# Optimization experiments

Hardware: AMD Instinct MI355X
Metric: run time of the kernel (lower is better)

Reference implementation:

```python
import jax, jax.numpy as jnp
import numpy as np

N, E = 50000, 800000
NFEAT, NHID, NCLASS = 128, 64, 40
GROUPS = 32  # min(32, nhid)
EPS = 1e-5


def _gcn(x, W, b, src, tgt, mvals):
    # GraphConvolution: linear, gather from src, weighted scatter-add to tgt
    s = x @ W + b                                  # [N, out]
    msg = s[src] * mvals[:, None]                   # [E, out]
    return jax.ops.segment_sum(msg, tgt, num_segments=N)


def _groupnorm(x, gamma, beta):
    n, c = x.shape
    xg = x.reshape(n, GROUPS, c // GROUPS)
    mu = jnp.mean(xg, axis=-1, keepdims=True)
    var = jnp.mean(jnp.square(xg - mu), axis=-1, keepdims=True)
    xn = ((xg - mu) * jax.lax.rsqrt(var + EPS)).reshape(n, c)
    return xn * gamma + beta


def setup_inputs() -> dict:
    key = jax.random.key(0)
    ks = jax.random.split(key, 16)
    x = jax.random.normal(ks[0], (N, NFEAT), dtype=jnp.float32)
    src = jax.random.randint(ks[1], (E,), 0, N, dtype=jnp.int64)
    tgt = jax.random.randint(ks[2], (E,), 0, N, dtype=jnp.int64)
    Mtgt = jax.random.uniform(ks[3], (E,), dtype=jnp.float32)

    def glorot(k, fin, fout):
        lim = np.sqrt(6.0 / (fin + fout))
        return jax.random.uniform(k, (fin, fout), jnp.float32, -lim, lim)

    return {
        "x": x, "src": src, "tgt": tgt, "Mtgt": Mtgt,
        "W0": glorot(ks[4], NFEAT, NHID), "b0": jnp.zeros((NHID,), jnp.float32),
        "W1": glorot(ks[5], NHID, NHID),  "b1": jnp.zeros((NHID,), jnp.float32),
        "W2": glorot(ks[6], NHID, NHID),  "b2": jnp.zeros((NHID,), jnp.float32),
        "W3": glorot(ks[7], NHID, NCLASS),"b3": jnp.zeros((NCLASS,), jnp.float32),
        "g1": jnp.ones((NHID,), jnp.float32), "beta1": jnp.zeros((NHID,), jnp.float32),
        "g2": jnp.ones((NHID,), jnp.float32), "beta2": jnp.zeros((NHID,), jnp.float32),
    }


def reference(x, src, tgt, Mtgt, W0, b0, W1, b1, W2, b2, W3, b3, g1, beta1, g2, beta2):
    # layer 0 + relu (dropout is identity in eval mode)
    h = jax.nn.relu(_gcn(x, W0, b0, src, tgt, Mtgt))
    # middle layers: residue_layers=1 -> each layer is its own residual block
    r = h
    h = _groupnorm(jax.nn.relu(_gcn(h, W1, b1, src, tgt, Mtgt)), g1, beta1) + r
    r = h
    h = _groupnorm(jax.nn.relu(_gcn(h, W2, b2, src, tgt, Mtgt)), g2, beta2) + r
    # output layer
    h = _gcn(h, W3, b3, src, tgt, Mtgt)
    return jax.nn.log_softmax(h, axis=1)
```

## Files before the change

kernel.cpp:

```cpp
#include <hip/hip_runtime.h>
#include <hip/hip_bf16.h>
#include <hip/hip_fp16.h>
#include <math.h>


#define EPS 1e-5f
#define ELLC 48
#define CPAD 4
#define NPART 8

__device__ inline unsigned pack_h2(float a, float b) {
    __half2 h = __floats2half2_rn(a, b);
    return *(unsigned*)&h;
}
__device__ inline float2 unpack_h2(unsigned u) {
    __half2 h = *(__half2*)&u;
    return __half22float2(h);
}
__device__ inline float h16f(unsigned short u) {
    __half h;
    *(unsigned short*)&h = u;
    return __half2float(h);
}

__global__ void fill_lin0_kernel(const int* __restrict__ src,
                                 const int* __restrict__ tgt,
                                 const float* __restrict__ mv,
                                 int* __restrict__ cntp,
                                 unsigned* __restrict__ ep, int E,
                                 const float* __restrict__ X,
                                 const float4* __restrict__ W4,
                                 const float4* __restrict__ B4,
                                 uint2* __restrict__ ShOut, int n, int psz,
                                 int fillBlocks, int halfBlocks) {
    __shared__ float4 Wl[128 * 8];
    __shared__ float4 Bl8[8];
    if (blockIdx.x < (unsigned)fillBlocks) {
        int part = blockIdx.x & (NPART - 1);
        int chunk = blockIdx.x >> 3;
        int e = chunk * blockDim.x + threadIdx.x;
        if (e >= E) return;
        int t = tgt[e];
        if ((unsigned)(t - part * psz) >= (unsigned)psz) return;
        int slot = atomicAdd(&cntp[t * CPAD], 1);
        if (slot < ELLC) {
            __half hw = __float2half_rn(mv[e]);
            unsigned v = (unsigned)src[e] |
                         ((unsigned)*(unsigned short*)&hw << 16);
            ep[(long)t * ELLC + slot] = v;
        }
        return;
    }
    int tb = blockIdx.x - fillBlocks;
    int half = (tb >= halfBlocks) ? 1 : 0;
    int bi = tb - half * halfBlocks;
    for (int i = threadIdx.x; i < 128 * 8; i += blockDim.x)
        Wl[i] = W4[(i >> 3) * 16 + half * 8 + (i & 7)];
    if (threadIdx.x < 8) Bl8[threadIdx.x] = B4[half * 8 + threadIdx.x];
    __syncthreads();
    int idx = bi * blockDim.x + threadIdx.x;
    if (idx >= n * 8) return;
    int row = idx >> 3;
    int c8 = idx & 7;
    const float* xr = X + (long)row * 128;
    float4 acc = Bl8[c8];
#pragma unroll 8
    for (int k = 0; k < 128; ++k) {
        float xv = xr[k];
        float4 w = Wl[k * 8 + c8];
        acc.x = fmaf(xv, w.x, acc.x);
        acc.y = fmaf(xv, w.y, acc.y);
        acc.z = fmaf(xv, w.z, acc.z);
        acc.w = fmaf(xv, w.w, acc.w);
    }
    ShOut[(long)row * 16 + half * 8 + c8] =
        make_uint2(pack_h2(acc.x, acc.y), pack_h2(acc.z, acc.w));
}

#define FMA4(A, V, W4)                                                        \
    A.x = fmaf(V.x, W4, A.x); A.y = fmaf(V.y, W4, A.y);                       \
    A.z = fmaf(V.z, W4, A.z); A.w = fmaf(V.w, W4, A.w);

#define HF_FMA(A, U, WV) {                                                    \
    float2 _lo = unpack_h2(U.x), _hi = unpack_h2(U.y);                        \
    A.x = fmaf(_lo.x, WV, A.x); A.y = fmaf(_lo.y, WV, A.y);                   \
    A.z = fmaf(_hi.x, WV, A.z); A.w = fmaf(_hi.y, WV, A.w); }

#define AGG4H_BODY(R2)                                                        \
    int beg = wid * ELLC;                                                     \
    int cnv = cntp[wid * CPAD];                                               \
    if (cnv > ELLC) cnv = ELLC;                                               \
    int end = beg + cnv;                                                      \
    float4 a0 = make_float4(0.f, 0.f, 0.f, 0.f), a1 = a0, a2 = a0, a3 = a0;   \
    int j = beg;                                                              \
    for (; j + 16 <= end; j += 16) {                                          \
        unsigned p0 = ep[j + q], p1 = ep[j + 4 + q];                          \
        unsigned p2 = ep[j + 8 + q], p3 = ep[j + 12 + q];                     \
        uint2 u0 = Sh[(long)(p0 & 0xFFFFu) * R2 + sub];                       \
        uint2 u1 = Sh[(long)(p1 & 0xFFFFu) * R2 + sub];                       \
        uint2 u2 = Sh[(long)(p2 & 0xFFFFu) * R2 + sub];                       \
        uint2 u3 = Sh[(long)(p3 & 0xFFFFu) * R2 + sub];                       \
        float w0 = h16f((unsigned short)(p0 >> 16));                          \
        float w1 = h16f((unsigned short)(p1 >> 16));                          \
        float w2 = h16f((unsigned short)(p2 >> 16));                          \
        float w3 = h16f((unsigned short)(p3 >> 16));                          \
        HF_FMA(a0, u0, w0) HF_FMA(a1, u1, w1)                                 \
        HF_FMA(a2, u2, w2) HF_FMA(a3, u3, w3)                                 \
    }                                                                         \
    for (; j + 4 <= end; j += 4) {                                            \
        unsigned p0 = ep[j + q];                                              \
        uint2 u0 = Sh[(long)(p0 & 0xFFFFu) * R2 + sub];                       \
        float w0 = h16f((unsigned short)(p0 >> 16));                          \
        HF_FMA(a0, u0, w0)                                                    \
    }                                                                         \
    if (j < end) {                                                            \
        int eidx = j + q;                                                     \
        unsigned p0 = ep[(eidx < end) ? eidx : (end - 1)];                    \
        uint2 u0 = Sh[(long)(p0 & 0xFFFFu) * R2 + sub];                       \
        float w0 = (eidx < end) ? h16f((unsigned short)(p0 >> 16)) : 0.f;     \
        HF_FMA(a0, u0, w0)                                                    \
    }                                                                         \
    float4 acc;                                                               \
    acc.x = (a0.x + a1.x) + (a2.x + a3.x);                                    \
    acc.y = (a0.y + a1.y) + (a2.y + a3.y);                                    \
    acc.z = (a0.z + a1.z) + (a2.z + a3.z);                                    \
    acc.w = (a0.w + a1.w) + (a2.w + a3.w);                                    \
    acc.x += __shfl_xor(acc.x, 16); acc.y += __shfl_xor(acc.y, 16);           \
    acc.z += __shfl_xor(acc.z, 16); acc.w += __shfl_xor(acc.w, 16);           \
    acc.x += __shfl_xor(acc.x, 32); acc.y += __shfl_xor(acc.y, 32);           \
    acc.z += __shfl_xor(acc.z, 32); acc.w += __shfl_xor(acc.w, 32);

#define LIN_TAIL_CORE(C4OUT)                                                  \
    float4 o = make_float4(0.f, 0.f, 0.f, 0.f);                               \
    {                                                                         \
        const float* hr = hrow[w];                                            \
        _Pragma("unroll")                                                     \
        for (int kk = 0; kk < 16; ++kk) {                                     \
            float hv = hr[16 * q + kk];                                       \
            float4 wv = Wl[(16 * q + kk) * C4OUT + sub];                      \
            FMA4(o, wv, hv)                                                   \
        }                                                                     \
        o.x += __shfl_xor(o.x, 16); o.y += __shfl_xor(o.y, 16);               \
        o.z += __shfl_xor(o.z, 16); o.w += __shfl_xor(o.w, 16);               \
        o.x += __shfl_xor(o.x, 32); o.y += __shfl_xor(o.y, 32);               \
        o.z += __shfl_xor(o.z, 32); o.w += __shfl_xor(o.w, 32);               \
    }

__global__ void agg_relu_lin_kernel(const uint2* __restrict__ Sh,
                                    const int* __restrict__ cntp,
                                    const unsigned* __restrict__ ep,
                                    const float4* __restrict__ W4,
                                    const float4* __restrict__ B4,
                                    float4* __restrict__ H4,
                                    uint2* __restrict__ ShOut, int n) {
    __shared__ float4 Wl[64 * 16];
    __shared__ float4 Bl[16];
    __shared__ float hrow[4][64];
    for (int i = threadIdx.x; i < 64 * 16; i += blockDim.x) Wl[i] = W4[i];
    if (threadIdx.x < 16) Bl[threadIdx.x] = B4[threadIdx.x];
    __syncthreads();
    int wid = (blockIdx.x * blockDim.x + threadIdx.x) >> 6;
    int lane = threadIdx.x & 63;
    int q = lane >> 4, sub = lane & 15;
    int w = threadIdx.x >> 6;
    if (wid >= n) return;
    AGG4H_BODY(16)
    if (q == 0) {
        float4 h = make_float4(fmaxf(acc.x, 0.f), fmaxf(acc.y, 0.f),
                               fmaxf(acc.z, 0.f), fmaxf(acc.w, 0.f));
        H4[(long)wid * 16 + sub] = h;
        ((float4*)hrow[w])[sub] = h;
    }
    LIN_TAIL_CORE(16)
    if (q == 0) {
        float4 b = Bl[sub];
        o.x += b.x; o.y += b.y; o.z += b.z; o.w += b.w;
        ShOut[(long)wid * 16 + sub] =
            make_uint2(pack_h2(o.x, o.y), pack_h2(o.z, o.w));
    }
}

template <int C4OUT>
__global__ void agg_gn_lin_kernel(const uint2* __restrict__ Sh,
                                  const int* __restrict__ cntp,
                                  const unsigned* __restrict__ ep,
                                  const float4* __restrict__ gamma,
                                  const float4* __restrict__ beta,
                                  const float4* __restrict__ W4,
                                  const float4* __restrict__ B4,
                                  float4* __restrict__ H4,
                                  uint2* __restrict__ ShOut, int n) {
    __shared__ float4 Wl[64 * C4OUT];
    __shared__ float4 Bl[C4OUT];
    __shared__ float hrow[4][64];
    for (int i = threadIdx.x; i < 64 * C4OUT; i += blockDim.x) Wl[i] = W4[i];
    if (threadIdx.x < C4OUT) Bl[threadIdx.x] = B4[threadIdx.x];
    __syncthreads();
    int wid = (blockIdx.x * blockDim.x + threadIdx.x) >> 6;
    int lane = threadIdx.x & 63;
    int q = lane >> 4, sub = lane & 15;
    int w = threadIdx.x >> 6;
    if (wid >= n) return;
    AGG4H_BODY(16)
    if (q == 0) {
        float p0 = fmaxf(acc.x, 0.f), p1 = fmaxf(acc.y, 0.f);
        float p2 = fmaxf(acc.z, 0.f), p3 = fmaxf(acc.w, 0.f);
        float dA = 0.5f * (p0 - p1);
        float dB = 0.5f * (p2 - p3);
        float rsA = rsqrtf(dA * dA + EPS);
        float rsB = rsqrtf(dB * dB + EPS);
        float4 g = gamma[sub], be = beta[sub];
        long off = (long)wid * 16 + sub;
        float4 h = H4[off];
        h.x += dA * rsA * g.x + be.x;
        h.y += -dA * rsA * g.y + be.y;
        h.z += dB * rsB * g.z + be.z;
        h.w += -dB * rsB * g.w + be.w;
        H4[off] = h;
        ((float4*)hrow[w])[sub] = h;
    }
    if (sub < C4OUT) {
        LIN_TAIL_CORE(C4OUT)
        if (q == 0) {
            float4 b = Bl[sub];
            o.x += b.x; o.y += b.y; o.z += b.z; o.w += b.w;
            ShOut[(long)wid * C4OUT + sub] =
                make_uint2(pack_h2(o.x, o.y), pack_h2(o.z, o.w));
        }
    }
}

__global__ void agg_lsm_kernel(const uint2* __restrict__ Sh,
                               const int* __restrict__ cntp,
                               const unsigned* __restrict__ ep,
                               float4* __restrict__ out4, int n) {
    int wid = (blockIdx.x * blockDim.x + threadIdx.x) >> 6;
    int lane = threadIdx.x & 63;
    int q = lane >> 4;
    int sub0 = lane & 15;
    int sub = (sub0 < 10) ? sub0 : 9;
    if (wid >= n) return;
    AGG4H_BODY(10)
    bool valid = sub0 < 10;
    float m = valid ? fmaxf(fmaxf(acc.x, acc.y), fmaxf(acc.z, acc.w)) : -INFINITY;
#pragma unroll
    for (int mk = 8; mk; mk >>= 1) m = fmaxf(m, __shfl_xor(m, mk));
    float ex = valid ? (expf(acc.x - m) + expf(acc.y - m) +
                        expf(acc.z - m) + expf(acc.w - m)) : 0.f;
#pragma unroll
    for (int mk = 8; mk; mk >>= 1) ex += __shfl_xor(ex, mk);
    float l = m + logf(ex);
    if (q == 0 && valid)
        out4[(long)wid * 10 + sub0] =
            make_float4(acc.x - l, acc.y - l, acc.z - l, acc.w - l);
}

extern "C" void kernel_launch(void* const* d_in, const int* in_sizes, int n_in,
                              void* d_out, int out_size, void* d_ws,
                              size_t ws_size, hipStream_t stream) {
    const float* x = (const float*)d_in[0];
    const int* src = (const int*)d_in[1];
    const int* tgt = (const int*)d_in[2];
    const float* mv = (const float*)d_in[3];
    const float* W0 = (const float*)d_in[4];
    const float* b0 = (const float*)d_in[5];
    const float* W1 = (const float*)d_in[6];
    const float* b1 = (const float*)d_in[7];
    const float* W2 = (const float*)d_in[8];
    const float* b2 = (const float*)d_in[9];
    const float* W3 = (const float*)d_in[10];
    const float* b3 = (const float*)d_in[11];
    const float* g1 = (const float*)d_in[12];
    const float* beta1 = (const float*)d_in[13];
    const float* g2 = (const float*)d_in[14];
    const float* beta2 = (const float*)d_in[15];

    const int N = in_sizes[0] / 128;
    const int E = in_sizes[1];

    uint2* bufA = (uint2*)d_ws;
    float* buf_h = (float*)(bufA + (size_t)N * 16);
    uint2* bufB = (uint2*)(buf_h + (size_t)N * 64);
    int* cntp = (int*)(bufB + (size_t)N * 16);
    unsigned* epack = (unsigned*)(((uintptr_t)(cntp + (size_t)N * CPAD) + 15) &
                                  ~(uintptr_t)15);

    const int BLK = 256;
    auto grid = [](long total, int blk) { return (int)((total + blk - 1) / blk); };
    const int chunkBlocks = grid(E, BLK);
    const int fillBlocks = NPART * chunkBlocks;
    const int halfBlocks = grid((long)N * 8, BLK);
    const int psz = (N + NPART - 1) / NPART;

    hipMemsetAsync(cntp, 0, (size_t)N * CPAD * sizeof(int), stream);
    fill_lin0_kernel<<<fillBlocks + 2 * halfBlocks, BLK, 0, stream>>>(
        src, tgt, mv, cntp, epack, E, x, (const float4*)W0, (const float4*)b0,
        bufA, N, psz, fillBlocks, halfBlocks);

    const int aggBlocks = grid((long)N * 64, BLK);

    agg_relu_lin_kernel<<<aggBlocks, BLK, 0, stream>>>(
        bufA, cntp, epack, (const float4*)W1, (const float4*)b1,
        (float4*)buf_h, bufB, N);

    agg_gn_lin_kernel<16><<<aggBlocks, BLK, 0, stream>>>(
        bufB, cntp, epack, (const float4*)g1, (const float4*)beta1,
        (const float4*)W2, (const float4*)b2, (float4*)buf_h, bufA, N);

    agg_gn_lin_kernel<10><<<aggBlocks, BLK, 0, stream>>>(
        bufA, cntp, epack, (const float4*)g2, (const float4*)beta2,
        (const float4*)W3, (const float4*)b3, (float4*)buf_h, bufB, N);

    agg_lsm_kernel<<<aggBlocks, BLK, 0, stream>>>(
        bufB, cntp, epack, (float4*)d_out, N);
}
```

Before: 298.3 us.

## Split 64-wide gather-aggregation into two column-half passes for cache locality

The fp16 node-feature tables are split into separate low and high 32-column halves, and each aggregation layer now runs as two kernels. Each kernel gathers only one half, so its random-access working set (about 3.2 MB) is more likely to stay cache-resident. The second pass fuses the GroupNorm/residual for its half and the following linear layer. The cost is extra kernel launches, a second traversal of the edge lists, and an extra read and write of H per layer.

Measured after the change: 343.2 us. +15.1%, slower.

```diff
diff --git a/kernel.cpp b/kernel.cpp
--- a/kernel.cpp
+++ b/kernel.cpp
@@ -1,5 +1,4 @@
 #include <hip/hip_runtime.h>
-#include <hip/hip_bf16.h>
 #include <hip/hip_fp16.h>
 #include <math.h>
 
@@ -22,6 +21,15 @@
     *(unsigned short*)&h = u;
     return __half2float(h);
 }
+
+#define FMA4(A, V, W4)                                                        \
+    A.x = fmaf(V.x, W4, A.x); A.y = fmaf(V.y, W4, A.y);                       \
+    A.z = fmaf(V.z, W4, A.z); A.w = fmaf(V.w, W4, A.w);
+
+#define HF_FMA(A, U, WV) {                                                    \
+    float2 _lo = unpack_h2(U.x), _hi = unpack_h2(U.y);                        \
+    A.x = fmaf(_lo.x, WV, A.x); A.y = fmaf(_lo.y, WV, A.y);                   \
+    A.z = fmaf(_hi.x, WV, A.z); A.w = fmaf(_hi.y, WV, A.w); }
 
 __global__ void fill_lin0_kernel(const int* __restrict__ src,
                                  const int* __restrict__ tgt,
@@ -31,7 +39,8 @@
                                  const float* __restrict__ X,
                                  const float4* __restrict__ W4,
                                  const float4* __restrict__ B4,
-                                 uint2* __restrict__ ShOut, int n, int psz,
+                                 uint2* __restrict__ S0lo,
+                                 uint2* __restrict__ S0hi, int n, int psz,
                                  int fillBlocks, int halfBlocks) {
     __shared__ float4 Wl[128 * 8];
     __shared__ float4 Bl8[8];
@@ -73,18 +82,168 @@
         acc.z = fmaf(xv, w.z, acc.z);
         acc.w = fmaf(xv, w.w, acc.w);
     }
-    ShOut[(long)row * 16 + half * 8 + c8] =
-        make_uint2(pack_h2(acc.x, acc.y), pack_h2(acc.z, acc.w));
-}
-
-#define FMA4(A, V, W4)                                                        \
-    A.x = fmaf(V.x, W4, A.x); A.y = fmaf(V.y, W4, A.y);                       \
-    A.z = fmaf(V.z, W4, A.z); A.w = fmaf(V.w, W4, A.w);
-
-#define HF_FMA(A, U, WV) {                                                    \
-    float2 _lo = unpack_h2(U.x), _hi = unpack_h2(U.y);                        \
-    A.x = fmaf(_lo.x, WV, A.x); A.y = fmaf(_lo.y, WV, A.y);                   \
-    A.z = fmaf(_hi.x, WV, A.z); A.w = fmaf(_hi.y, WV, A.w); }
+    uint2 v2 = make_uint2(pack_h2(acc.x, acc.y), pack_h2(acc.z, acc.w));
+    if (half) S0hi[(long)row * 8 + c8] = v2;
+    else      S0lo[(long)row * 8 + c8] = v2;
+}
+
+#define AGGH_BODY()                                                           \
+    int beg = wid * ELLC;                                                     \
+    int cnv = cntp[wid * CPAD];                                               \
+    if (cnv > ELLC) cnv = ELLC;                                               \
+    int end = beg + cnv;                                                      \
+    float4 a0 = make_float4(0.f, 0.f, 0.f, 0.f), a1 = a0;                     \
+    int j = beg;                                                              \
+    for (; j + 16 <= end; j += 16) {                                          \
+        unsigned p0 = ep[j + o], p1 = ep[j + 8 + o];                          \
+        uint2 u0 = Sh[(long)(p0 & 0xFFFFu) * 8 + sub];                        \
+        uint2 u1 = Sh[(long)(p1 & 0xFFFFu) * 8 + sub];                        \
+        float w0 = h16f((unsigned short)(p0 >> 16));                          \
+        float w1 = h16f((unsigned short)(p1 >> 16));                          \
+        HF_FMA(a0, u0, w0) HF_FMA(a1, u1, w1)                                 \
+    }                                                                         \
+    for (; j + 8 <= end; j += 8) {                                            \
+        unsigned p0 = ep[j + o];                                              \
+        uint2 u0 = Sh[(long)(p0 & 0xFFFFu) * 8 + sub];                        \
+        float w0 = h16f((unsigned short)(p0 >> 16));                          \
+        HF_FMA(a0, u0, w0)                                                    \
+    }                                                                         \
+    if (j < end) {                                                            \
+        int eidx = j + o;                                                     \
+        unsigned p0 = ep[(eidx < end) ? eidx : (end - 1)];                    \
+        uint2 u0 = Sh[(long)(p0 & 0xFFFFu) * 8 + sub];                        \
+        float w0 = (eidx < end) ? h16f((unsigned short)(p0 >> 16)) : 0.f;     \
+        HF_FMA(a0, u0, w0)                                                    \
+    }                                                                         \
+    float4 acc;                                                               \
+    acc.x = a0.x + a1.x; acc.y = a0.y + a1.y;                                 \
+    acc.z = a0.z + a1.z; acc.w = a0.w + a1.w;                                 \
+    acc.x += __shfl_xor(acc.x, 8);  acc.y += __shfl_xor(acc.y, 8);            \
+    acc.z += __shfl_xor(acc.z, 8);  acc.w += __shfl_xor(acc.w, 8);            \
+    acc.x += __shfl_xor(acc.x, 16); acc.y += __shfl_xor(acc.y, 16);           \
+    acc.z += __shfl_xor(acc.z, 16); acc.w += __shfl_xor(acc.w, 16);           \
+    acc.x += __shfl_xor(acc.x, 32); acc.y += __shfl_xor(acc.y, 32);           \
+    acc.z += __shfl_xor(acc.z, 32); acc.w += __shfl_xor(acc.w, 32);
+
+__global__ void aggA_relu_kernel(const uint2* __restrict__ Sh,
+                                 const int* __restrict__ cntp,
+                                 const unsigned* __restrict__ ep,
+                                 float4* __restrict__ H4, int n) {
+    int wid = (blockIdx.x * blockDim.x + threadIdx.x) >> 6;
+    int lane = threadIdx.x & 63;
+    int o = lane >> 3, sub = lane & 7;
+    if (wid >= n) return;
+    AGGH_BODY()
+    if (o == 0)
+        H4[(long)wid * 16 + sub] =
+            make_float4(fmaxf(acc.x, 0.f), fmaxf(acc.y, 0.f),
+                        fmaxf(acc.z, 0.f), fmaxf(acc.w, 0.f));
+}
+
+__global__ void aggA_gn_kernel(const uint2* __restrict__ Sh,
+                               const int* __restrict__ cntp,
+                               const unsigned* __restrict__ ep,
+                               const float4* __restrict__ gamma4,
+                               const float4* __restrict__ beta4,
+                               float4* __restrict__ H4, int n) {
+    int wid = (blockIdx.x * blockDim.x + threadIdx.x) >> 6;
+    int lane = threadIdx.x & 63;
+    int o = lane >> 3, sub = lane & 7;
+    if (wid >= n) return;
+    AGGH_BODY()
+    if (o == 0) {
+        float p0 = fmaxf(acc.x, 0.f), p1 = fmaxf(acc.y, 0.f);
+        float p2 = fmaxf(acc.z, 0.f), p3 = fmaxf(acc.w, 0.f);
+        float dA = 0.5f * (p0 - p1);
+        float dB = 0.5f * (p2 - p3);
+        float rsA = rsqrtf(dA * dA + EPS);
+        float rsB = rsqrtf(dB * dB + EPS);
+        float4 g = gamma4[sub], be = beta4[sub];
+        long off = (long)wid * 16 + sub;
+        float4 h = H4[off];
+        h.x += dA * rsA * g.x + be.x;
+        h.y += -dA * rsA * g.y + be.y;
+        h.z += dB * rsB * g.z + be.z;
+        h.w += -dB * rsB * g.w + be.w;
+        H4[off] = h;
+    }
+}
+
+template <int C4OUT, bool SPLIT, bool DOGN>
+__global__ void aggB_kernel(const uint2* __restrict__ Sh,
+                            const int* __restrict__ cntp,
+                            const unsigned* __restrict__ ep,
+                            const float4* __restrict__ gamma4h,
+                            const float4* __restrict__ beta4h,
+                            const float4* __restrict__ W4,
+                            const float4* __restrict__ B4,
+                            float4* __restrict__ H4,
+                            uint2* __restrict__ OutLo,
+                            uint2* __restrict__ OutHi, int n) {
+    __shared__ float4 Wl[64 * C4OUT];
+    __shared__ float4 Bl[C4OUT];
+    __shared__ float hrow[4][64];
+    for (int i = threadIdx.x; i < 64 * C4OUT; i += blockDim.x) Wl[i] = W4[i];
+    if (threadIdx.x < C4OUT) Bl[threadIdx.x] = B4[threadIdx.x];
+    __syncthreads();
+    int wid = (blockIdx.x * blockDim.x + threadIdx.x) >> 6;
+    int lane = threadIdx.x & 63;
+    int o = lane >> 3, sub = lane & 7;
+    int w = threadIdx.x >> 6;
+    if (wid >= n) return;
+    AGGH_BODY()
+    if (o == 1)
+        ((float4*)hrow[w])[sub] = H4[(long)wid * 16 + sub];
+    if (o == 0) {
+        float4 h;
+        long off = (long)wid * 16 + 8 + sub;
+        if (DOGN) {
+            float p0 = fmaxf(acc.x, 0.f), p1 = fmaxf(acc.y, 0.f);
+            float p2 = fmaxf(acc.z, 0.f), p3 = fmaxf(acc.w, 0.f);
+            float dA = 0.5f * (p0 - p1);
+            float dB = 0.5f * (p2 - p3);
+            float rsA = rsqrtf(dA * dA + EPS);
+            float rsB = rsqrtf(dB * dB + EPS);
+            float4 g = gamma4h[sub], be = beta4h[sub];
+            h = H4[off];
+            h.x += dA * rsA * g.x + be.x;
+            h.y += -dA * rsA * g.y + be.y;
+            h.z += dB * rsB * g.z + be.z;
+            h.w += -dB * rsB * g.w + be.w;
+        } else {
+            h = make_float4(fmaxf(acc.x, 0.f), fmaxf(acc.y, 0.f),
+                            fmaxf(acc.z, 0.f), fmaxf(acc.w, 0.f));
+        }
+        H4[off] = h;
+        ((float4*)hrow[w])[8 + sub] = h;
+    }
+    int q16 = lane >> 4, s16 = lane & 15;
+    if (C4OUT == 16 || s16 < C4OUT) {
+        float4 oo = make_float4(0.f, 0.f, 0.f, 0.f);
+        const float* hr = hrow[w];
+#pragma unroll
+        for (int kk = 0; kk < 16; ++kk) {
+            float hv = hr[16 * q16 + kk];
+            float4 wv = Wl[(16 * q16 + kk) * C4OUT + s16];
+            FMA4(oo, wv, hv)
+        }
+        oo.x += __shfl_xor(oo.x, 16); oo.y += __shfl_xor(oo.y, 16);
+        oo.z += __shfl_xor(oo.z, 16); oo.w += __shfl_xor(oo.w, 16);
+        oo.x += __shfl_xor(oo.x, 32); oo.y += __shfl_xor(oo.y, 32);
+        oo.z += __shfl_xor(oo.z, 32); oo.w += __shfl_xor(oo.w, 32);
+        if (q16 == 0) {
+            float4 b = Bl[s16];
+            oo.x += b.x; oo.y += b.y; oo.z += b.z; oo.w += b.w;
+            uint2 v2 = make_uint2(pack_h2(oo.x, oo.y), pack_h2(oo.z, oo.w));
+            if (SPLIT) {
+                if (s16 < 8) OutLo[(long)wid * 8 + s16] = v2;
+                else         OutHi[(long)wid * 8 + (s16 - 8)] = v2;
+            } else {
+                OutLo[(long)wid * C4OUT + s16] = v2;
+            }
+        }
+    }
+}
 
 #define AGG4H_BODY(R2)                                                        \
     int beg = wid * ELLC;                                                     \
@@ -129,106 +288,6 @@
     acc.z += __shfl_xor(acc.z, 16); acc.w += __shfl_xor(acc.w, 16);           \
     acc.x += __shfl_xor(acc.x, 32); acc.y += __shfl_xor(acc.y, 32);           \
     acc.z += __shfl_xor(acc.z, 32); acc.w += __shfl_xor(acc.w, 32);
-
-#define LIN_TAIL_CORE(C4OUT)                                                  \
-    float4 o = make_float4(0.f, 0.f, 0.f, 0.f);                               \
-    {                                                                         \
-        const float* hr = hrow[w];                                            \
-        _Pragma("unroll")                                                     \
-        for (int kk = 0; kk < 16; ++kk) {                                     \
-            float hv = hr[16 * q + kk];                                       \
-            float4 wv = Wl[(16 * q + kk) * C4OUT + sub];                      \
-            FMA4(o, wv, hv)                                                   \
-        }                                                                     \
-        o.x += __shfl_xor(o.x, 16); o.y += __shfl_xor(o.y, 16);               \
-        o.z += __shfl_xor(o.z, 16); o.w += __shfl_xor(o.w, 16);               \
-        o.x += __shfl_xor(o.x, 32); o.y += __shfl_xor(o.y, 32);               \
-        o.z += __shfl_xor(o.z, 32); o.w += __shfl_xor(o.w, 32);               \
-    }
-
-__global__ void agg_relu_lin_kernel(const uint2* __restrict__ Sh,
-                                    const int* __restrict__ cntp,
-                                    const unsigned* __restrict__ ep,
-                                    const float4* __restrict__ W4,
-                                    const float4* __restrict__ B4,
-                                    float4* __restrict__ H4,
-                                    uint2* __restrict__ ShOut, int n) {
-    __shared__ float4 Wl[64 * 16];
-    __shared__ float4 Bl[16];
-    __shared__ float hrow[4][64];
-    for (int i = threadIdx.x; i < 64 * 16; i += blockDim.x) Wl[i] = W4[i];
-    if (threadIdx.x < 16) Bl[threadIdx.x] = B4[threadIdx.x];
-    __syncthreads();
-    int wid = (blockIdx.x * blockDim.x + threadIdx.x) >> 6;
-    int lane = threadIdx.x & 63;
-    int q = lane >> 4, sub = lane & 15;
-    int w = threadIdx.x >> 6;
-    if (wid >= n) return;
-    AGG4H_BODY(16)
-    if (q == 0) {
-        float4 h = make_float4(fmaxf(acc.x, 0.f), fmaxf(acc.y, 0.f),
-                               fmaxf(acc.z, 0.f), fmaxf(acc.w, 0.f));
-        H4[(long)wid * 16 + sub] = h;
-        ((float4*)hrow[w])[sub] = h;
-    }
-    LIN_TAIL_CORE(16)
-    if (q == 0) {
-        float4 b = Bl[sub];
-        o.x += b.x; o.y += b.y; o.z += b.z; o.w += b.w;
-        ShOut[(long)wid * 16 + sub] =
-            make_uint2(pack_h2(o.x, o.y), pack_h2(o.z, o.w));
-    }
-}
-
-template <int C4OUT>
-__global__ void agg_gn_lin_kernel(const uint2* __restrict__ Sh,
-                                  const int* __restrict__ cntp,
-                                  const unsigned* __restrict__ ep,
-                                  const float4* __restrict__ gamma,
-                                  const float4* __restrict__ beta,
-                                  const float4* __restrict__ W4,
-                                  const float4* __restrict__ B4,
-                                  float4* __restrict__ H4,
-                                  uint2* __restrict__ ShOut, int n) {
-    __shared__ float4 Wl[64 * C4OUT];
-    __shared__ float4 Bl[C4OUT];
-    __shared__ float hrow[4][64];
-    for (int i = threadIdx.x; i < 64 * C4OUT; i += blockDim.x) Wl[i] = W4[i];
-    if (threadIdx.x < C4OUT) Bl[threadIdx.x] = B4[threadIdx.x];
-    __syncthreads();
-    int wid = (blockIdx.x * blockDim.x + threadIdx.x) >> 6;
-    int lane = threadIdx.x & 63;
-    int q = lane >> 4, sub = lane & 15;
-    int w = threadIdx.x >> 6;
-    if (wid >= n) return;
-    AGG4H_BODY(16)
-    if (q == 0) {
-        float p0 = fmaxf(acc.x, 0.f), p1 = fmaxf(acc.y, 0.f);
-        float p2 = fmaxf(acc.z, 0.f), p3 = fmaxf(acc.w, 0.f);
-        float dA = 0.5f * (p0 - p1);
-        float dB = 0.5f * (p2 - p3);
-        float rsA = rsqrtf(dA * dA + EPS);
-        float rsB = rsqrtf(dB * dB + EPS);
-        float4 g = gamma[sub], be = beta[sub];
-        long off = (long)wid * 16 + sub;
-        float4 h = H4[off];
-        h.x += dA * rsA * g.x + be.x;
-        h.y += -dA * rsA * g.y + be.y;
-        h.z += dB * rsB * g.z + be.z;
-        h.w += -dB * rsB * g.w + be.w;
-        H4[off] = h;
-        ((float4*)hrow[w])[sub] = h;
-    }
-    if (sub < C4OUT) {
-        LIN_TAIL_CORE(C4OUT)
-        if (q == 0) {
-            float4 b = Bl[sub];
-            o.x += b.x; o.y += b.y; o.z += b.z; o.w += b.w;
-            ShOut[(long)wid * C4OUT + sub] =
-                make_uint2(pack_h2(o.x, o.y), pack_h2(o.z, o.w));
-        }
-    }
-}
 
 __global__ void agg_lsm_kernel(const uint2* __restrict__ Sh,
                                const int* __restrict__ cntp,
@@ -278,10 +337,14 @@
     const int N = in_sizes[0] / 128;
     const int E = in_sizes[1];
 
-    uint2* bufA = (uint2*)d_ws;
-    float* buf_h = (float*)(bufA + (size_t)N * 16);
-    uint2* bufB = (uint2*)(buf_h + (size_t)N * 64);
-    int* cntp = (int*)(bufB + (size_t)N * 16);
+    uint2* regA = (uint2*)d_ws;
+    uint2* S0lo = regA;
+    uint2* S0hi = regA + (size_t)N * 8;
+    float* buf_h = (float*)(regA + (size_t)N * 16);
+    uint2* regB = (uint2*)(buf_h + (size_t)N * 64);
+    uint2* S1lo = regB;
+    uint2* S1hi = regB + (size_t)N * 8;
+    int* cntp = (int*)(regB + (size_t)N * 16);
     unsigned* epack = (unsigned*)(((uintptr_t)(cntp + (size_t)N * CPAD) + 15) &
                                   ~(uintptr_t)15);
 
@@ -295,22 +358,32 @@
     hipMemsetAsync(cntp, 0, (size_t)N * CPAD * sizeof(int), stream);
     fill_lin0_kernel<<<fillBlocks + 2 * halfBlocks, BLK, 0, stream>>>(
         src, tgt, mv, cntp, epack, E, x, (const float4*)W0, (const float4*)b0,
-        bufA, N, psz, fillBlocks, halfBlocks);
+        S0lo, S0hi, N, psz, fillBlocks, halfBlocks);
 
     const int aggBlocks = grid((long)N * 64, BLK);
-
-    agg_relu_lin_kernel<<<aggBlocks, BLK, 0, stream>>>(
-        bufA, cntp, epack, (const float4*)W1, (const float4*)b1,
-        (float4*)buf_h, bufB, N);
-
-    agg_gn_lin_kernel<16><<<aggBlocks, BLK, 0, stream>>>(
-        bufB, cntp, epack, (const float4*)g1, (const float4*)beta1,
-        (const float4*)W2, (const float4*)b2, (float4*)buf_h, bufA, N);
-
-    agg_gn_lin_kernel<10><<<aggBlocks, BLK, 0, stream>>>(
-        bufA, cntp, epack, (const float4*)g2, (const float4*)beta2,
-        (const float4*)W3, (const float4*)b3, (float4*)buf_h, bufB, N);
-
-    agg_lsm_kernel<<<aggBlocks, BLK, 0, stream>>>(
-        bufB, cntp, epack, (float4*)d_out, N);
-}
+    const float4* g1f = (const float4*)g1;
+    const float4* be1f = (const float4*)beta1;
+    const float4* g2f = (const float4*)g2;
+    const float4* be2f = (const float4*)beta2;
+
+    aggA_relu_kernel<<<aggBlocks, BLK, 0, stream>>>(S0lo, cntp, epack,
+                                                    (float4*)buf_h, N);
+    aggB_kernel<16, true, false><<<aggBlocks, BLK, 0, stream>>>(
+        S0hi, cntp, epack, nullptr, nullptr, (const float4*)W1,
+        (const float4*)b1, (float4*)buf_h, S1lo, S1hi, N);
+
+    aggA_gn_kernel<<<aggBlocks, BLK, 0, stream>>>(S1lo, cntp, epack, g1f, be1f,
+                                                  (float4*)buf_h, N);
+    aggB_kernel<16, true, true><<<aggBlocks, BLK, 0, stream>>>(
+        S1hi, cntp, epack, g1f + 8, be1f + 8, (const float4*)W2,
+        (const float4*)b2, (float4*)buf_h, S0lo, S0hi, N);
+
+    aggA_gn_kernel<<<aggBlocks, BLK, 0, stream>>>(S0lo, cntp, epack, g2f, be2f,
+                                                  (float4*)buf_h, N);
+    aggB_kernel<10, false, true><<<aggBlocks, BLK, 0, stream>>>(
+        S0hi, cntp, epack, g2f + 8, be2f + 8, (const float4*)W3,
+        (const float4*)b3, (float4*)buf_h, regB, nullptr, N);
+
+    agg_lsm_kernel<<<aggBlocks, BLK, 0, stream>>>(regB, cntp, epack,
+                                                  (float4*)d_out, N);
+}
```
